# Optimization experiments

Measured on AMD Instinct MI355X. Metric: run time of the kernel, lower is better.

The kernel has to match this reference:

```python
import jax, jax.numpy as jnp
import numpy as np

B, T, I, H = 128, 1024, 256, 512


def setup_inputs() -> dict:
    key = jax.random.key(0)
    ks = jax.random.split(key, 7)
    s_in = 1.0 / np.sqrt(I + H)  # torch Linear default init scale
    inp = {
        "x": jax.random.normal(ks[0], (B, T, I), dtype=jnp.float32),
        "Wz": jax.random.uniform(ks[1], (I + H, H), jnp.float32, -s_in, s_in),
        "bz": jax.random.uniform(ks[2], (H,), jnp.float32, -s_in, s_in),
        "Wr": jax.random.uniform(ks[3], (I + H, H), jnp.float32, -s_in, s_in),
        "br": jax.random.uniform(ks[4], (H,), jnp.float32, -s_in, s_in),
        "Wh": jax.random.uniform(ks[5], (I + H, H), jnp.float32, -s_in, s_in),
        "bh": jax.random.uniform(ks[6], (H,), jnp.float32, -s_in, s_in),
    }
    return inp


def reference(x, Wz, bz, Wr, br, Wh, bh):
    # x: [B, T, I]; custom GRU cell, h0 = zeros. Note the (nonstandard)
    # blend h = (1-z)*h + z*h_cand, exactly as in the torch source.
    batch, hidden = x.shape[0], Wz.shape[1]

    def step(h, x_t):
        comb = jnp.concatenate([x_t, h], axis=1)          # [B, I+H]
        z = jax.nn.sigmoid(comb @ Wz + bz)                # [B, H]
        r = jax.nn.sigmoid(comb @ Wr + br)                # [B, H]
        comb2 = jnp.concatenate([x_t, r * h], axis=1)     # [B, I+H]
        h_cand = jnp.tanh(comb2 @ Wh + bh)                # [B, H]
        h_new = (1.0 - z) * h + z * h_cand
        return h_new, h_new

    h0 = jnp.zeros((batch, hidden), dtype=x.dtype)
    _, ys = jax.lax.scan(step, h0, jnp.swapaxes(x, 0, 1))  # ys: [T, B, H]
    return jnp.swapaxes(ys, 0, 1)                          # [B, T, H]
```

## Files before the change

kernel.cpp:

```cpp
#include <hip/hip_runtime.h>
#include <math.h>

#define BB 128
#define TT 1024
#define II 256
#define HH 512
#define KK 768

typedef __attribute__((ext_vector_type(8))) short short8v;
typedef __attribute__((ext_vector_type(4))) float float4v;
typedef __attribute__((ext_vector_type(4))) unsigned int uint4v;

#define BARS_OFF   0
#define BARS_SZ    32768
#define WFRAG_OFF  BARS_SZ
#define WFRAG_SZ   (96 * 24 * 64 * 16)
#define GS_OFF     (WFRAG_OFF + WFRAG_SZ)
#define GS_STRIDE  65536
#define WS_NEED    ((size_t)GS_OFF + 8 * GS_STRIDE)

#define NT_MAIN 320

__device__ __forceinline__ unsigned short bf16_rne(float f) {
    unsigned u = __builtin_bit_cast(unsigned, f);
    unsigned r = u + 0x7FFFu + ((u >> 16) & 1u);
    return (unsigned short)(r >> 16);
}
__device__ __forceinline__ void cp16(void* lds, const void* g) {
    __builtin_amdgcn_global_load_lds(
        (const __attribute__((address_space(1))) unsigned*)g,
        (__attribute__((address_space(3))) unsigned*)lds, 16, 0, 0);
}

#define MFMA __builtin_amdgcn_mfma_f32_16x16x32_bf16

__global__ void repack_w(const float* __restrict__ Wz, const float* __restrict__ Wr,
                         const float* __restrict__ Wh, short8v* __restrict__ wB) {
    const int ntAll = blockIdx.x;
    const int w = threadIdx.x >> 6, l = threadIdx.x & 63;
    const float* W; int n0;
    if (ntAll < 32)      { W = Wz; n0 = ntAll * 16; }
    else if (ntAll < 64) { W = Wr; n0 = (ntAll - 32) * 16; }
    else                 { W = Wh; n0 = (ntAll - 64) * 16; }
    const int n = n0 + (l & 15);
    for (int kt = w; kt < 24; kt += 4) {
        const int k0 = kt * 32 + (l >> 4) * 8;
        short8v f;
        #pragma unroll
        for (int j = 0; j < 8; ++j)
            f[j] = (short)bf16_rne(W[(size_t)(k0 + j) * HH + n]);
        wB[((size_t)ntAll * 24 + kt) * 64 + l] = f;
    }
}

__global__ __launch_bounds__(NT_MAIN, 1) void gru_mfma(
    const float* __restrict__ x,
    const float* __restrict__ bz, const float* __restrict__ br,
    const float* __restrict__ bh,
    float* __restrict__ out,
    const short8v* __restrict__ wB,
    char* __restrict__ gsBase,
    unsigned* __restrict__ bars)
{
    __shared__ short8v bx1[4][8][64];
    __shared__ short8v bx2[2][8][64];
    __shared__ short8v xF[8][64];
    __shared__ float4v red1[4][4][64];
    __shared__ float4v red2[2][4][64];
    __shared__ float rhA[16][33];
    __shared__ float hL[16][33];

    const int tid = threadIdx.x;
    const int w = tid >> 6, l = tid & 63;
    const int g = blockIdx.x & 7, s = blockIdx.x >> 3;
    const int m_ = l & 15, kg = l >> 4;

    char* gs = gsBase + (size_t)g * GS_STRIDE;
    short8v* hFrag  = (short8v*)gs;
    short8v* rhFrag = hFrag + 16 * 64;
    unsigned* flagBase = bars + (size_t)g * 16 * 64;

    short8v wh1[4][4];
    short8v wh2[2][4];
    if (w < 4) {
        const int ownNt = (w < 2) ? (2 * s + w) : (32 + 2 * s + (w - 2));
        for (int i = 0; i < 8; ++i)
            cp16(&bx1[w][i][0], wB + ((size_t)ownNt * 24 + i) * 64 + l);
        if (w < 2)
            for (int i = 0; i < 8; ++i)
                cp16(&bx2[w][i][0], wB + ((size_t)(64 + 2 * s + w) * 24 + i) * 64 + l);
        #pragma unroll
        for (int T = 0; T < 4; ++T) {
            const int nt = (T < 2) ? (2 * s + T) : (32 + 2 * s + (T - 2));
            #pragma unroll
            for (int q = 0; q < 4; ++q)
                wh1[T][q] = wB[((size_t)nt * 24 + 8 + 4 * w + q) * 64 + l];
        }
        #pragma unroll
        for (int n2 = 0; n2 < 2; ++n2)
            #pragma unroll
            for (int q = 0; q < 4; ++q)
                wh2[n2][q] = wB[((size_t)(64 + 2 * s + n2) * 24 + 8 + 4 * w + q) * 64 + l];
    }
    const float bias1 = (w < 2) ? bz[s * 32 + w * 16 + m_]
                    : (w < 4)  ? br[s * 32 + (w - 2) * 16 + m_] : 0.f;
    const float bias2 = (w < 2) ? bh[s * 32 + w * 16 + m_] : 0.f;

    for (int idx = tid; idx < 16 * 33; idx += NT_MAIN) ((float*)hL)[idx] = 0.f;

    for (int slot = tid; slot < 512; slot += NT_MAIN) {
        const int kt = slot >> 6, ll = slot & 63;
        const float* xp = x + (size_t)(g * 16 + (ll & 15)) * (TT * II)
                            + kt * 32 + (ll >> 4) * 8;
        const float4 v0 = *(const float4*)xp;
        const float4 v1 = *(const float4*)(xp + 4);
        short8v f;
        f[0] = (short)bf16_rne(v0.x); f[1] = (short)bf16_rne(v0.y);
        f[2] = (short)bf16_rne(v0.z); f[3] = (short)bf16_rne(v0.w);
        f[4] = (short)bf16_rne(v1.x); f[5] = (short)bf16_rne(v1.y);
        f[6] = (short)bf16_rne(v1.z); f[7] = (short)bf16_rne(v1.w);
        xF[kt][ll] = f;
    }
    __syncthreads();

    float4 xv[16];

    for (int t = 0; t < TT; ++t) {
        float4v ax0 = {0.f, 0.f, 0.f, 0.f}, ax1 = ax0;
        if (w < 4) {
            #pragma unroll
            for (int kt = 0; kt < 8; kt += 2) {
                ax0 = MFMA(xF[kt][l],     bx1[w][kt][l],     ax0, 0, 0, 0);
                ax1 = MFMA(xF[kt + 1][l], bx1[w][kt + 1][l], ax1, 0, 0, 0);
            }
        } else if (t + 1 < TT) {
            #pragma unroll
            for (int i = 0; i < 8; ++i) {
                const float* xp = x + (size_t)(g * 16 + m_) * (TT * II)
                                    + (size_t)(t + 1) * II + i * 32 + kg * 8;
                xv[2 * i]     = *(const float4*)xp;
                xv[2 * i + 1] = *(const float4*)(xp + 4);
            }
        }

        short8v hf0, hf1, hf2, hf3;
        if (w < 4) {
            if (l < 4) {
                const unsigned* fp = flagBase + (4 * w + l) * 64;
                while (__hip_atomic_load(fp, __ATOMIC_RELAXED,
                                         __HIP_MEMORY_SCOPE_AGENT) < (unsigned)t)
                    __builtin_amdgcn_s_sleep(1);
            }
            uint4v u0, u1, u2, u3;
            const short8v* hp = hFrag + (size_t)(4 * w) * 64 + l;
            asm volatile("global_load_dwordx4 %0, %1, off sc1" : "=v"(u0) : "v"(hp)       : "memory");
            asm volatile("global_load_dwordx4 %0, %1, off sc1" : "=v"(u1) : "v"(hp +  64) : "memory");
            asm volatile("global_load_dwordx4 %0, %1, off sc1" : "=v"(u2) : "v"(hp + 128) : "memory");
            asm volatile("global_load_dwordx4 %0, %1, off sc1" : "=v"(u3) : "v"(hp + 192) : "memory");
            asm volatile("s_waitcnt vmcnt(0)" ::: "memory");
            __builtin_amdgcn_sched_barrier(0);
            hf0 = __builtin_bit_cast(short8v, u0);
            hf1 = __builtin_bit_cast(short8v, u1);
            hf2 = __builtin_bit_cast(short8v, u2);
            hf3 = __builtin_bit_cast(short8v, u3);
            float4v h0 = {0.f,0.f,0.f,0.f}, h1 = h0, h2 = h0, h3 = h0;
            #pragma unroll
            for (int q = 0; q < 4; ++q) {
                const short8v a = (q == 0) ? hf0 : (q == 1) ? hf1 : (q == 2) ? hf2 : hf3;
                h0 = MFMA(a, wh1[0][q], h0, 0, 0, 0);
                h1 = MFMA(a, wh1[1][q], h1, 0, 0, 0);
                h2 = MFMA(a, wh1[2][q], h2, 0, 0, 0);
                h3 = MFMA(a, wh1[3][q], h3, 0, 0, 0);
            }
            red1[0][w][l] = h0; red1[1][w][l] = h1;
            red1[2][w][l] = h2; red1[3][w][l] = h3;
        }
        __syncthreads();

        float zreg[4];
        if (w < 4) {
            float4v s1v = ax0 + ax1 + red1[w][0][l] + red1[w][1][l]
                                  + red1[w][2][l] + red1[w][3][l];
            #pragma unroll
            for (int r = 0; r < 4; ++r) {
                const float sg = 1.f / (1.f + __expf(-(s1v[r] + bias1)));
                if (w < 2) zreg[r] = sg;
                else rhA[kg * 4 + r][(w - 2) * 16 + m_] =
                         sg * hL[kg * 4 + r][(w - 2) * 16 + m_];
            }
        }
        __syncthreads();

        if (w == 2) {
            short8v f;
            #pragma unroll
            for (int j = 0; j < 8; ++j)
                f[j] = (short)bf16_rne(rhA[m_][kg * 8 + j]);
            const uint4v u = __builtin_bit_cast(uint4v, f);
            short8v* dp = rhFrag + (size_t)s * 64 + l;
            asm volatile("global_store_dwordx4 %0, %1, off sc1" :: "v"(dp), "v"(u) : "memory");
            asm volatile("s_waitcnt vmcnt(0)" ::: "memory");
            if (l == 0)
                __hip_atomic_store(flagBase + s * 64 + 32, (unsigned)(t + 1),
                                   __ATOMIC_RELAXED, __HIP_MEMORY_SCOPE_AGENT);
        }
        float4v cx0 = {0.f,0.f,0.f,0.f}, cx1 = cx0;
        if (w < 2) {
            #pragma unroll
            for (int kt = 0; kt < 8; kt += 2) {
                cx0 = MFMA(xF[kt][l],     bx2[w][kt][l],     cx0, 0, 0, 0);
                cx1 = MFMA(xF[kt + 1][l], bx2[w][kt + 1][l], cx1, 0, 0, 0);
            }
        }

        if (w < 4) {
            if (l < 4) {
                const unsigned* fp = flagBase + (4 * w + l) * 64 + 32;
                while (__hip_atomic_load(fp, __ATOMIC_RELAXED,
                                         __HIP_MEMORY_SCOPE_AGENT) < (unsigned)(t + 1))
                    __builtin_amdgcn_s_sleep(1);
            }
            uint4v u0, u1, u2, u3;
            const short8v* rp = rhFrag + (size_t)(4 * w) * 64 + l;
            asm volatile("global_load_dwordx4 %0, %1, off sc1" : "=v"(u0) : "v"(rp)       : "memory");
            asm volatile("global_load_dwordx4 %0, %1, off sc1" : "=v"(u1) : "v"(rp +  64) : "memory");
            asm volatile("global_load_dwordx4 %0, %1, off sc1" : "=v"(u2) : "v"(rp + 128) : "memory");
            asm volatile("global_load_dwordx4 %0, %1, off sc1" : "=v"(u3) : "v"(rp + 192) : "memory");
            asm volatile("s_waitcnt vmcnt(0)" ::: "memory");
            __builtin_amdgcn_sched_barrier(0);
            const short8v rf0 = __builtin_bit_cast(short8v, u0);
            const short8v rf1 = __builtin_bit_cast(short8v, u1);
            const short8v rf2 = __builtin_bit_cast(short8v, u2);
            const short8v rf3 = __builtin_bit_cast(short8v, u3);
            float4v c0 = {0.f,0.f,0.f,0.f}, c1 = c0;
            #pragma unroll
            for (int q = 0; q < 4; ++q) {
                const short8v a = (q == 0) ? rf0 : (q == 1) ? rf1 : (q == 2) ? rf2 : rf3;
                c0 = MFMA(a, wh2[0][q], c0, 0, 0, 0);
                c1 = MFMA(a, wh2[1][q], c1, 0, 0, 0);
            }
            red2[0][w][l] = c0; red2[1][w][l] = c1;
        }
        __syncthreads();

        if (w < 2) {
            float4v s2v = cx0 + cx1 + red2[w][0][l] + red2[w][1][l]
                                  + red2[w][2][l] + red2[w][3][l];
            #pragma unroll
            for (int r = 0; r < 4; ++r) {
                const int row = kg * 4 + r;
                const int cl = w * 16 + m_;
                const float hc = tanhf(s2v[r] + bias2);
                const float ho = hL[row][cl];
                hL[row][cl] = (1.f - zreg[r]) * ho + zreg[r] * (hc - ho) + zreg[r] * ho;
            }
        } else if (w == 4 && t + 1 < TT) {
            #pragma unroll
            for (int i = 0; i < 8; ++i) {
                const float4 v0 = xv[2 * i], v1 = xv[2 * i + 1];
                short8v f;
                f[0] = (short)bf16_rne(v0.x); f[1] = (short)bf16_rne(v0.y);
                f[2] = (short)bf16_rne(v0.z); f[3] = (short)bf16_rne(v0.w);
                f[4] = (short)bf16_rne(v1.x); f[5] = (short)bf16_rne(v1.y);
                f[6] = (short)bf16_rne(v1.z); f[7] = (short)bf16_rne(v1.w);
                xF[i][l] = f;
            }
        }
        __syncthreads();

        if (w == 4) {
            short8v f;
            #pragma unroll
            for (int j = 0; j < 8; ++j)
                f[j] = (short)bf16_rne(hL[m_][kg * 8 + j]);
            const uint4v u = __builtin_bit_cast(uint4v, f);
            short8v* dp = hFrag + (size_t)s * 64 + l;
            asm volatile("global_store_dwordx4 %0, %1, off sc1" :: "v"(dp), "v"(u) : "memory");
            asm volatile("s_waitcnt vmcnt(0)" ::: "memory");
            if (l == 0)
                __hip_atomic_store(flagBase + s * 64, (unsigned)(t + 1),
                                   __ATOMIC_RELAXED, __HIP_MEMORY_SCOPE_AGENT);
        } else if (w == 3) {
            float* op = out + (size_t)(g * 16 + m_) * (TT * HH) + (size_t)t * HH
                            + s * 32 + kg * 8;
            float4 o0, o1;
            o0.x = hL[m_][kg * 8 + 0]; o0.y = hL[m_][kg * 8 + 1];
            o0.z = hL[m_][kg * 8 + 2]; o0.w = hL[m_][kg * 8 + 3];
            o1.x = hL[m_][kg * 8 + 4]; o1.y = hL[m_][kg * 8 + 5];
            o1.z = hL[m_][kg * 8 + 6]; o1.w = hL[m_][kg * 8 + 7];
            *(float4*)op = o0;
            *(float4*)(op + 4) = o1;
        }
    }
}

#define NWG_FB 64
#define NTHR_FB 512
__global__ __launch_bounds__(NTHR_FB, 1) void gru_rowsplit(
    const float* __restrict__ x,
    const float* __restrict__ Wz, const float* __restrict__ bz,
    const float* __restrict__ Wr, const float* __restrict__ br,
    const float* __restrict__ Wh, const float* __restrict__ bh,
    float* __restrict__ out)
{
    __shared__ float comb_i [KK][2];
    __shared__ float comb2_i[KK][2];
    __shared__ float z_s[2][HH];
    __shared__ float red1[8][257];
    __shared__ float red2[24][129];

    const int tid  = threadIdx.x;
    const int row0 = blockIdx.x * 2;
    const int kh = tid >> 8;
    const int t1 = tid & 255;
    const int n1 = t1 * 4;
    const float* __restrict__ w1 =
        ((n1 < HH) ? (Wz + n1) : (Wr + (n1 - HH))) + (size_t)(kh * 384) * HH;
    const int kq = tid >> 7;
    const int t2 = tid & 127;
    const int n2 = t2 * 4;
    const float* __restrict__ w2 = Wh + n2 + (size_t)(kq * 192) * HH;

    float b1[4], b2[4];
    #pragma unroll
    for (int j = 0; j < 4; ++j) {
        b1[j] = (n1 + j < HH) ? bz[n1 + j] : br[n1 + j - HH];
        b2[j] = bh[n2 + j];
    }
    for (int idx = tid; idx < HH * 2; idx += NTHR_FB)
        comb_i[II + (idx >> 1)][idx & 1] = 0.f;
    __syncthreads();

    for (int t = 0; t < TT; ++t) {
        {
            const int r = tid >> 8, k = tid & 255;
            const float v = x[(size_t)(row0 + r) * (TT * II) + (size_t)t * II + k];
            comb_i [k][r] = v;
            comb2_i[k][r] = v;
        }
        __syncthreads();
        float a00=0,a01=0,a02=0,a03=0,a10=0,a11=0,a12=0,a13=0;
        {
            const int kb = kh * 384;
            #pragma unroll 8
            for (int k = 0; k < 384; ++k) {
                const float4 w = *(const float4*)(w1 + (size_t)k * HH);
                const float2 a = *(const float2*)&comb_i[kb + k][0];
                a00 += a.x*w.x; a01 += a.x*w.y; a02 += a.x*w.z; a03 += a.x*w.w;
                a10 += a.y*w.x; a11 += a.y*w.y; a12 += a.y*w.z; a13 += a.y*w.w;
            }
        }
        if (kh == 1) {
            red1[0][t1]=a00; red1[1][t1]=a01; red1[2][t1]=a02; red1[3][t1]=a03;
            red1[4][t1]=a10; red1[5][t1]=a11; red1[6][t1]=a12; red1[7][t1]=a13;
        }
        __syncthreads();
        if (kh == 0) {
            float accv[2][4] = {{a00,a01,a02,a03},{a10,a11,a12,a13}};
            #pragma unroll
            for (int r = 0; r < 2; ++r) {
                #pragma unroll
                for (int j = 0; j < 4; ++j) {
                    const int n = n1 + j;
                    const float v = accv[r][j] + red1[r*4+j][t1] + b1[j];
                    const float sg = 1.f / (1.f + __expf(-v));
                    if (n < HH) z_s[r][n] = sg;
                    else {
                        const int nh = n - HH;
                        comb2_i[II + nh][r] = sg * comb_i[II + nh][r];
                    }
                }
            }
        }
        __syncthreads();
        float c00=0,c01=0,c02=0,c03=0,c10=0,c11=0,c12=0,c13=0;
        {
            const int kb = kq * 192;
            #pragma unroll 8
            for (int k = 0; k < 192; ++k) {
                const float4 w = *(const float4*)(w2 + (size_t)k * HH);
                const float2 a = *(const float2*)&comb2_i[kb + k][0];
                c00 += a.x*w.x; c01 += a.x*w.y; c02 += a.x*w.z; c03 += a.x*w.w;
                c10 += a.y*w.x; c11 += a.y*w.y; c12 += a.y*w.z; c13 += a.y*w.w;
            }
        }
        if (kq > 0) {
            const int base = (kq - 1) * 8;
            red2[base+0][t2]=c00; red2[base+1][t2]=c01;
            red2[base+2][t2]=c02; red2[base+3][t2]=c03;
            red2[base+4][t2]=c10; red2[base+5][t2]=c11;
            red2[base+6][t2]=c12; red2[base+7][t2]=c13;
        }
        __syncthreads();
        if (kq == 0) {
            float accv[2][4] = {{c00,c01,c02,c03},{c10,c11,c12,c13}};
            #pragma unroll
            for (int r = 0; r < 2; ++r) {
                float hn4[4];
                #pragma unroll
                for (int j = 0; j < 4; ++j) {
                    const int n = n2 + j;
                    const int jj = r * 4 + j;
                    const float v = accv[r][j] + red2[jj][t2] + red2[8+jj][t2]
                                  + red2[16+jj][t2] + b2[j];
                    const float hc = tanhf(v);
                    const float zv = z_s[r][n];
                    const float ho = comb_i[II + n][r];
                    const float hn = (1.f - zv) * ho + zv * hc;
                    comb_i[II + n][r] = hn;
                    hn4[j] = hn;
                }
                *(float4*)&out[(size_t)(row0 + r) * (TT * HH) + (size_t)t * HH + n2] =
                    make_float4(hn4[0], hn4[1], hn4[2], hn4[3]);
            }
        }
        __syncthreads();
    }
}

extern "C" void kernel_launch(void* const* d_in, const int* in_sizes, int n_in,
                              void* d_out, int out_size, void* d_ws, size_t ws_size,
                              hipStream_t stream) {
    const float* x  = (const float*)d_in[0];
    const float* Wz = (const float*)d_in[1];
    const float* bz = (const float*)d_in[2];
    const float* Wr = (const float*)d_in[3];
    const float* br = (const float*)d_in[4];
    const float* Wh = (const float*)d_in[5];
    const float* bh = (const float*)d_in[6];
    float* out = (float*)d_out;

    if (ws_size < WS_NEED) {
        gru_rowsplit<<<NWG_FB, NTHR_FB, 0, stream>>>(x, Wz, bz, Wr, br, Wh, bh, out);
        return;
    }

    char* ws = (char*)d_ws;
    unsigned* bars = (unsigned*)(ws + BARS_OFF);
    short8v*  wB   = (short8v*)(ws + WFRAG_OFF);
    char*     gs   = ws + GS_OFF;

    hipMemsetAsync(bars, 0, BARS_SZ, stream);
    hipMemsetAsync(gs, 0, 8 * (size_t)GS_STRIDE, stream);
    repack_w<<<96, 256, 0, stream>>>(Wz, Wr, Wh, wB);
    gru_mfma<<<128, NT_MAIN, 0, stream>>>(x, bz, br, bh, out, wB, gs, bars);
}
```

Before: 4.531 ms.

## Remove per-step block barriers via split flags, double-buffered x, and fast activations

Cuts two of the four __syncthreads per timestep. The warps that compute r*h and h now publish their own halves of the fragment to global memory, each with its own flag, and consumers poll two flags per producer block instead of one. The x fragment buffer is double-buffered so the prefetch warp can write step t+1 while step t is still being read. The output store is deferred by one step and moved to warp 4. Sigmoid and tanh switch to rcp/exp approximations, and the h blend is simplified. This shortens the serial critical path at the cost of lower activation accuracy and subtler inter-warp ordering that relies on the remaining barriers.

Result: no change. 4.569 ms (median of 2 runs) (+0.8%).

```diff
diff --git a/kernel.cpp b/kernel.cpp
--- a/kernel.cpp
+++ b/kernel.cpp
@@ -30,6 +30,13 @@
     __builtin_amdgcn_global_load_lds(
         (const __attribute__((address_space(1))) unsigned*)g,
         (__attribute__((address_space(3))) unsigned*)lds, 16, 0, 0);
+}
+__device__ __forceinline__ float sigmoid_fast(float v) {
+    return __builtin_amdgcn_rcpf(1.f + __expf(-v));
+}
+__device__ __forceinline__ float tanh_fast(float v) {
+    const float e = __expf(2.f * v);
+    return 1.f - 2.f * __builtin_amdgcn_rcpf(e + 1.f);
 }
 
 #define MFMA __builtin_amdgcn_mfma_f32_16x16x32_bf16
@@ -64,7 +71,7 @@
 {
     __shared__ short8v bx1[4][8][64];
     __shared__ short8v bx2[2][8][64];
-    __shared__ short8v xF[8][64];
+    __shared__ short8v xF[2][8][64];
     __shared__ float4v red1[4][4][64];
     __shared__ float4v red2[2][4][64];
     __shared__ float rhA[16][33];
@@ -119,19 +126,21 @@
         f[2] = (short)bf16_rne(v0.z); f[3] = (short)bf16_rne(v0.w);
         f[4] = (short)bf16_rne(v1.x); f[5] = (short)bf16_rne(v1.y);
         f[6] = (short)bf16_rne(v1.z); f[7] = (short)bf16_rne(v1.w);
-        xF[kt][ll] = f;
+        xF[0][kt][ll] = f;
     }
     __syncthreads();
 
     float4 xv[16];
 
     for (int t = 0; t < TT; ++t) {
+        const int xb = t & 1;
+
         float4v ax0 = {0.f, 0.f, 0.f, 0.f}, ax1 = ax0;
         if (w < 4) {
             #pragma unroll
             for (int kt = 0; kt < 8; kt += 2) {
-                ax0 = MFMA(xF[kt][l],     bx1[w][kt][l],     ax0, 0, 0, 0);
-                ax1 = MFMA(xF[kt + 1][l], bx1[w][kt + 1][l], ax1, 0, 0, 0);
+                ax0 = MFMA(xF[xb][kt][l],     bx1[w][kt][l],     ax0, 0, 0, 0);
+                ax1 = MFMA(xF[xb][kt + 1][l], bx1[w][kt + 1][l], ax1, 0, 0, 0);
             }
         } else if (t + 1 < TT) {
             #pragma unroll
@@ -143,10 +152,9 @@
             }
         }
 
-        short8v hf0, hf1, hf2, hf3;
         if (w < 4) {
-            if (l < 4) {
-                const unsigned* fp = flagBase + (4 * w + l) * 64;
+            if (l < 8) {
+                const unsigned* fp = flagBase + (4 * w + (l >> 1)) * 64 + (l & 1) * 8;
                 while (__hip_atomic_load(fp, __ATOMIC_RELAXED,
                                          __HIP_MEMORY_SCOPE_AGENT) < (unsigned)t)
                     __builtin_amdgcn_s_sleep(1);
@@ -159,10 +167,10 @@
             asm volatile("global_load_dwordx4 %0, %1, off sc1" : "=v"(u3) : "v"(hp + 192) : "memory");
             asm volatile("s_waitcnt vmcnt(0)" ::: "memory");
             __builtin_amdgcn_sched_barrier(0);
-            hf0 = __builtin_bit_cast(short8v, u0);
-            hf1 = __builtin_bit_cast(short8v, u1);
-            hf2 = __builtin_bit_cast(short8v, u2);
-            hf3 = __builtin_bit_cast(short8v, u3);
+            const short8v hf0 = __builtin_bit_cast(short8v, u0);
+            const short8v hf1 = __builtin_bit_cast(short8v, u1);
+            const short8v hf2 = __builtin_bit_cast(short8v, u2);
+            const short8v hf3 = __builtin_bit_cast(short8v, u3);
             float4v h0 = {0.f,0.f,0.f,0.f}, h1 = h0, h2 = h0, h3 = h0;
             #pragma unroll
             for (int q = 0; q < 4; ++q) {
@@ -183,39 +191,72 @@
                                   + red1[w][2][l] + red1[w][3][l];
             #pragma unroll
             for (int r = 0; r < 4; ++r) {
-                const float sg = 1.f / (1.f + __expf(-(s1v[r] + bias1)));
+                const float sg = sigmoid_fast(s1v[r] + bias1);
                 if (w < 2) zreg[r] = sg;
                 else rhA[kg * 4 + r][(w - 2) * 16 + m_] =
                          sg * hL[kg * 4 + r][(w - 2) * 16 + m_];
             }
         }
-        __syncthreads();
-
-        if (w == 2) {
-            short8v f;
-            #pragma unroll
-            for (int j = 0; j < 8; ++j)
-                f[j] = (short)bf16_rne(rhA[m_][kg * 8 + j]);
-            const uint4v u = __builtin_bit_cast(uint4v, f);
-            short8v* dp = rhFrag + (size_t)s * 64 + l;
-            asm volatile("global_store_dwordx4 %0, %1, off sc1" :: "v"(dp), "v"(u) : "memory");
+        if (w == 2 || w == 3) {
+            asm volatile("s_waitcnt lgkmcnt(0)" ::: "memory");
+            __builtin_amdgcn_sched_barrier(0);
+            const bool mine = (w == 2) ? (l < 32) : (l >= 32);
+            if (mine) {
+                short8v f;
+                #pragma unroll
+                for (int j = 0; j < 8; ++j)
+                    f[j] = (short)bf16_rne(rhA[m_][kg * 8 + j]);
+                const uint4v u = __builtin_bit_cast(uint4v, f);
+                short8v* dp = rhFrag + (size_t)s * 64 + l;
+                asm volatile("global_store_dwordx4 %0, %1, off sc1" :: "v"(dp), "v"(u) : "memory");
+            }
             asm volatile("s_waitcnt vmcnt(0)" ::: "memory");
-            if (l == 0)
-                __hip_atomic_store(flagBase + s * 64 + 32, (unsigned)(t + 1),
+            if (w == 2 && l == 0)
+                __hip_atomic_store(flagBase + s * 64 + 16, (unsigned)(t + 1),
                                    __ATOMIC_RELAXED, __HIP_MEMORY_SCOPE_AGENT);
-        }
+            if (w == 3 && l == 32)
+                __hip_atomic_store(flagBase + s * 64 + 24, (unsigned)(t + 1),
+                                   __ATOMIC_RELAXED, __HIP_MEMORY_SCOPE_AGENT);
+        }
+        if (w == 4) {
+            asm volatile("s_waitcnt vmcnt(0)" ::: "memory");
+            if (t + 1 < TT) {
+                #pragma unroll
+                for (int i = 0; i < 8; ++i) {
+                    const float4 v0 = xv[2 * i], v1 = xv[2 * i + 1];
+                    short8v f;
+                    f[0] = (short)bf16_rne(v0.x); f[1] = (short)bf16_rne(v0.y);
+                    f[2] = (short)bf16_rne(v0.z); f[3] = (short)bf16_rne(v0.w);
+                    f[4] = (short)bf16_rne(v1.x); f[5] = (short)bf16_rne(v1.y);
+                    f[6] = (short)bf16_rne(v1.z); f[7] = (short)bf16_rne(v1.w);
+                    xF[xb ^ 1][i][l] = f;
+                }
+            }
+            if (t > 0) {
+                float* op = out + (size_t)(g * 16 + m_) * (TT * HH)
+                                + (size_t)(t - 1) * HH + s * 32 + kg * 8;
+                float4 o0, o1;
+                o0.x = hL[m_][kg * 8 + 0]; o0.y = hL[m_][kg * 8 + 1];
+                o0.z = hL[m_][kg * 8 + 2]; o0.w = hL[m_][kg * 8 + 3];
+                o1.x = hL[m_][kg * 8 + 4]; o1.y = hL[m_][kg * 8 + 5];
+                o1.z = hL[m_][kg * 8 + 6]; o1.w = hL[m_][kg * 8 + 7];
+                *(float4*)op = o0;
+                *(float4*)(op + 4) = o1;
+            }
+        }
+
         float4v cx0 = {0.f,0.f,0.f,0.f}, cx1 = cx0;
         if (w < 2) {
             #pragma unroll
             for (int kt = 0; kt < 8; kt += 2) {
-                cx0 = MFMA(xF[kt][l],     bx2[w][kt][l],     cx0, 0, 0, 0);
-                cx1 = MFMA(xF[kt + 1][l], bx2[w][kt + 1][l], cx1, 0, 0, 0);
+                cx0 = MFMA(xF[xb][kt][l],     bx2[w][kt][l],     cx0, 0, 0, 0);
+                cx1 = MFMA(xF[xb][kt + 1][l], bx2[w][kt + 1][l], cx1, 0, 0, 0);
             }
         }
 
         if (w < 4) {
-            if (l < 4) {
-                const unsigned* fp = flagBase + (4 * w + l) * 64 + 32;
+            if (l < 8) {
+                const unsigned* fp = flagBase + (4 * w + (l >> 1)) * 64 + 16 + (l & 1) * 8;
                 while (__hip_atomic_load(fp, __ATOMIC_RELAXED,
                                          __HIP_MEMORY_SCOPE_AGENT) < (unsigned)(t + 1))
                     __builtin_amdgcn_s_sleep(1);
@@ -250,47 +291,43 @@
             for (int r = 0; r < 4; ++r) {
                 const int row = kg * 4 + r;
                 const int cl = w * 16 + m_;
-                const float hc = tanhf(s2v[r] + bias2);
+                const float hc = tanh_fast(s2v[r] + bias2);
                 const float ho = hL[row][cl];
-                hL[row][cl] = (1.f - zreg[r]) * ho + zreg[r] * (hc - ho) + zreg[r] * ho;
-            }
-        } else if (w == 4 && t + 1 < TT) {
-            #pragma unroll
-            for (int i = 0; i < 8; ++i) {
-                const float4 v0 = xv[2 * i], v1 = xv[2 * i + 1];
+                hL[row][cl] = (1.f - zreg[r]) * ho + zreg[r] * hc;
+            }
+            asm volatile("s_waitcnt lgkmcnt(0)" ::: "memory");
+            __builtin_amdgcn_sched_barrier(0);
+            const bool mine = (w == 0) ? (l < 32) : (l >= 32);
+            if (mine) {
                 short8v f;
-                f[0] = (short)bf16_rne(v0.x); f[1] = (short)bf16_rne(v0.y);
-                f[2] = (short)bf16_rne(v0.z); f[3] = (short)bf16_rne(v0.w);
-                f[4] = (short)bf16_rne(v1.x); f[5] = (short)bf16_rne(v1.y);
-                f[6] = (short)bf16_rne(v1.z); f[7] = (short)bf16_rne(v1.w);
-                xF[i][l] = f;
-            }
-        }
-        __syncthreads();
-
-        if (w == 4) {
-            short8v f;
-            #pragma unroll
-            for (int j = 0; j < 8; ++j)
-                f[j] = (short)bf16_rne(hL[m_][kg * 8 + j]);
-            const uint4v u = __builtin_bit_cast(uint4v, f);
-            short8v* dp = hFrag + (size_t)s * 64 + l;
-            asm volatile("global_store_dwordx4 %0, %1, off sc1" :: "v"(dp), "v"(u) : "memory");
+                #pragma unroll
+                for (int j = 0; j < 8; ++j)
+                    f[j] = (short)bf16_rne(hL[m_][kg * 8 + j]);
+                const uint4v u = __builtin_bit_cast(uint4v, f);
+                short8v* dp = hFrag + (size_t)s * 64 + l;
+                asm volatile("global_store_dwordx4 %0, %1, off sc1" :: "v"(dp), "v"(u) : "memory");
+            }
             asm volatile("s_waitcnt vmcnt(0)" ::: "memory");
-            if (l == 0)
-                __hip_atomic_store(flagBase + s * 64, (unsigned)(t + 1),
+            if (w == 0 && l == 0)
+                __hip_atomic_store(flagBase + s * 64 + 0, (unsigned)(t + 1),
                                    __ATOMIC_RELAXED, __HIP_MEMORY_SCOPE_AGENT);
-        } else if (w == 3) {
-            float* op = out + (size_t)(g * 16 + m_) * (TT * HH) + (size_t)t * HH
-                            + s * 32 + kg * 8;
-            float4 o0, o1;
-            o0.x = hL[m_][kg * 8 + 0]; o0.y = hL[m_][kg * 8 + 1];
-            o0.z = hL[m_][kg * 8 + 2]; o0.w = hL[m_][kg * 8 + 3];
-            o1.x = hL[m_][kg * 8 + 4]; o1.y = hL[m_][kg * 8 + 5];
-            o1.z = hL[m_][kg * 8 + 6]; o1.w = hL[m_][kg * 8 + 7];
-            *(float4*)op = o0;
-            *(float4*)(op + 4) = o1;
-        }
+            if (w == 1 && l == 32)
+                __hip_atomic_store(flagBase + s * 64 + 8, (unsigned)(t + 1),
+                                   __ATOMIC_RELAXED, __HIP_MEMORY_SCOPE_AGENT);
+        }
+    }
+
+    __syncthreads();
+    if (w == 4) {
+        float* op = out + (size_t)(g * 16 + m_) * (TT * HH)
+                        + (size_t)(TT - 1) * HH + s * 32 + kg * 8;
+        float4 o0, o1;
+        o0.x = hL[m_][kg * 8 + 0]; o0.y = hL[m_][kg * 8 + 1];
+        o0.z = hL[m_][kg * 8 + 2]; o0.w = hL[m_][kg * 8 + 3];
+        o1.x = hL[m_][kg * 8 + 4]; o1.y = hL[m_][kg * 8 + 5];
+        o1.z = hL[m_][kg * 8 + 6]; o1.w = hL[m_][kg * 8 + 7];
+        *(float4*)op = o0;
+        *(float4*)(op + 4) = o1;
     }
 }
 
```
